# Performance work log

Hardware: AMD Instinct MI355X
Metric: run time of the kernel (lower is better)

Reference implementation:

```python
import jax, jax.numpy as jnp
import numpy as np

N_NODES = 100000
N_EDGES = 1000000
NUM_FEATURES = 64
HIDDEN = 64
NUM_GRAPHS = 128


def setup_inputs() -> dict:
    key = jax.random.key(0)
    ks = jax.random.split(key, 12)
    x = jax.random.normal(ks[0], (N_NODES, NUM_FEATURES), dtype=jnp.float32)
    edge_index = jax.random.randint(ks[1], (2, N_EDGES), 0, N_NODES, dtype=jnp.int64)
    edge_weight = jax.random.uniform(ks[2], (N_EDGES,), dtype=jnp.float32)
    batch = jnp.sort(jax.random.randint(ks[3], (N_NODES,), 0, NUM_GRAPHS, dtype=jnp.int64))
    s1 = 1.0 / np.sqrt(NUM_FEATURES)
    s2 = 1.0 / np.sqrt(HIDDEN)
    # GraphConv layer 1: lin_rel (with bias) applied to aggregated msgs, lin_root (no bias)
    w1_rel = jax.random.uniform(ks[4], (HIDDEN, NUM_FEATURES), jnp.float32, -s1, s1)
    b1_rel = jax.random.uniform(ks[5], (HIDDEN,), jnp.float32, -s1, s1)
    w1_root = jax.random.uniform(ks[6], (HIDDEN, NUM_FEATURES), jnp.float32, -s1, s1)
    # GraphConv layer 2
    w2_rel = jax.random.uniform(ks[7], (HIDDEN, HIDDEN), jnp.float32, -s2, s2)
    b2_rel = jax.random.uniform(ks[8], (HIDDEN,), jnp.float32, -s2, s2)
    w2_root = jax.random.uniform(ks[9], (HIDDEN, HIDDEN), jnp.float32, -s2, s2)
    # final Linear(hidden, 1)
    w_lin = jax.random.uniform(ks[10], (1, HIDDEN), jnp.float32, -s2, s2)
    b_lin = jax.random.uniform(ks[11], (1,), jnp.float32, -s2, s2)
    return {
        "x": x, "edge_index": edge_index, "edge_weight": edge_weight, "batch": batch,
        "w1_rel": w1_rel, "b1_rel": b1_rel, "w1_root": w1_root,
        "w2_rel": w2_rel, "b2_rel": b2_rel, "w2_root": w2_root,
        "w_lin": w_lin, "b_lin": b_lin,
    }


def graph_conv(x, edge_index, edge_weight, w_rel, b_rel, w_root):
    # messages: x[src] * e, scatter-add into dst  (gather-scale-scatter)
    src, dst = edge_index[0], edge_index[1]
    msgs = x[src] * edge_weight[:, None]                      # [E, F]
    aggr = jax.ops.segment_sum(msgs, dst, num_segments=x.shape[0])  # [N, F]
    return aggr @ w_rel.T + b_rel + x @ w_root.T


def reference(x, edge_index, edge_weight, batch,
              w1_rel, b1_rel, w1_root, w2_rel, b2_rel, w2_root, w_lin, b_lin):
    h = graph_conv(x, edge_index, edge_weight, w1_rel, b1_rel, w1_root)
    h = jax.nn.relu(h)
    h = graph_conv(h, edge_index, edge_weight, w2_rel, b2_rel, w2_root)
    # global_mean_pool over graph ids
    sums = jax.ops.segment_sum(h, batch, num_segments=NUM_GRAPHS)          # [G, H]
    counts = jax.ops.segment_sum(jnp.ones((h.shape[0],), h.dtype), batch,
                                 num_segments=NUM_GRAPHS)                  # [G]
    pooled = sums / jnp.maximum(counts, 1.0)[:, None]
    # dropout(p=0.5) in eval mode is identity
    return pooled @ w_lin.T + b_lin                                        # [G, 1]
```

## Files before the change

kernel.cpp:

```cpp
#include <hip/hip_runtime.h>
#include <hip/hip_bf16.h>


#define N_NODES 100000
#define N_EDGES 1000000
#define NGRAPHS 128
#define BN 512
#define NBUCK ((N_NODES + BN - 1) / BN)
#define FILL_T 16
#define FILL_TILE (256 * FILL_T)
#define FILL_NB ((N_EDGES + FILL_TILE - 1) / FILL_TILE)
#define NTILES (N_NODES / 16)
#define AST 72

typedef __attribute__((ext_vector_type(8))) short bf16x8;
typedef __attribute__((ext_vector_type(8))) unsigned short u16x8;
typedef __attribute__((ext_vector_type(4))) float f32x4;

__device__ __forceinline__ unsigned short f2bf(float f) {
    unsigned u = __float_as_uint(f);
    unsigned r = (u + 0x7FFFu + ((u >> 16) & 1u)) >> 16;
    return (unsigned short)r;
}
__device__ __forceinline__ float bf2f(unsigned short h) {
    return __uint_as_float(((unsigned)h) << 16);
}

__global__ __launch_bounds__(256) void prep_cvt_kernel(
    const float* __restrict__ x, unsigned short* __restrict__ xh, int n8,
    const float* __restrict__ w1rel, const float* __restrict__ w1root,
    const float* __restrict__ w2rel, const float* __restrict__ w2root,
    const float* __restrict__ wlin, const float* __restrict__ b2rel,
    const float* __restrict__ blin, unsigned short* __restrict__ whirel,
    unsigned short* __restrict__ wlorel, unsigned short* __restrict__ whiroot,
    unsigned short* __restrict__ wloroot, float* __restrict__ u,
    float* __restrict__ v, float* __restrict__ C) {
    int tid = threadIdx.x;
    int i = blockIdx.x * 256 + tid;
    if (i < n8) {
        const float4* xp = (const float4*)x + (size_t)i * 2;
        float4 a = xp[0], b = xp[1];
        u16x8 o;
        o[0] = f2bf(a.x); o[1] = f2bf(a.y); o[2] = f2bf(a.z); o[3] = f2bf(a.w);
        o[4] = f2bf(b.x); o[5] = f2bf(b.y); o[6] = f2bf(b.z); o[7] = f2bf(b.w);
        *((u16x8*)xh + i) = o;
        return;
    }
    for (int k = tid; k < 4096; k += 256) {
        float a = w1rel[k];
        unsigned short hi = f2bf(a);
        whirel[k] = hi;
        wlorel[k] = f2bf(a - bf2f(hi));
        float b = w1root[k];
        unsigned short hb = f2bf(b);
        whiroot[k] = hb;
        wloroot[k] = f2bf(b - bf2f(hb));
    }
    if (tid < 64) {
        float uu = 0.f, vv = 0.f;
        for (int h = 0; h < 64; ++h) {
            float wl = wlin[h];
            uu += wl * w2rel[h * 64 + tid];
            vv += wl * w2root[h * 64 + tid];
        }
        u[tid] = uu;
        v[tid] = vv;
    }
    if (tid == 0) {
        float c = blin[0];
        for (int h = 0; h < 64; ++h) c += wlin[h] * b2rel[h];
        *C = c;
    }
}

__global__ __launch_bounds__(256) void bucket_hist(const int* __restrict__ ei,
                                                   int* __restrict__ bcount,
                                                   int E) {
    __shared__ int lh[NBUCK];
    int tid = threadIdx.x;
    for (int i = tid; i < NBUCK; i += 256) lh[i] = 0;
    __syncthreads();
    for (int e = blockIdx.x * 256 + tid; e < E; e += gridDim.x * 256)
        atomicAdd(&lh[ei[E + e] >> 9], 1);
    __syncthreads();
    for (int i = tid; i < NBUCK; i += 256) {
        int c = lh[i];
        if (c) atomicAdd(&bcount[i], c);
    }
}

__global__ void bucket_scan(const int* __restrict__ bcount,
                            int* __restrict__ boff, int* __restrict__ cursor) {
    __shared__ int s[256];
    int t = threadIdx.x;
    int v = (t < NBUCK) ? bcount[t] : 0;
    s[t] = v;
    __syncthreads();
    for (int off = 1; off < 256; off <<= 1) {
        int x = (t >= off) ? s[t - off] : 0;
        __syncthreads();
        s[t] += x;
        __syncthreads();
    }
    if (t < NBUCK) {
        boff[t] = s[t] - v;
        cursor[t] = s[t] - v;
    }
    if (t == 255) boff[NBUCK] = s[255];
}

__global__ __launch_bounds__(256) void bucket_fill(
    const int* __restrict__ ei, const float* __restrict__ ew,
    int* __restrict__ cursor, int2* __restrict__ ebuf, int E) {
    __shared__ int lh[NBUCK];
    __shared__ int gbase[NBUCK];
    int tid = threadIdx.x;
    for (int i = tid; i < NBUCK; i += 256) lh[i] = 0;
    __syncthreads();
    int base = blockIdx.x * FILL_TILE;
    int2 rec[FILL_T];
    int meta[FILL_T];
#pragma unroll
    for (int i = 0; i < FILL_T; ++i) {
        int e = base + i * 256 + tid;
        meta[i] = -1;
        if (e < E) {
            int src = ei[e];
            int dst = ei[E + e];
            int b = dst >> 9;
            int r = atomicAdd(&lh[b], 1);
            rec[i].x = src | ((dst & (BN - 1)) << 17);
            rec[i].y = __float_as_int(ew[e]);
            meta[i] = (b << 13) | r;
        }
    }
    __syncthreads();
    for (int i = tid; i < NBUCK; i += 256) {
        int c = lh[i];
        gbase[i] = c ? atomicAdd(&cursor[i], c) : 0;
    }
    __syncthreads();
#pragma unroll
    for (int i = 0; i < FILL_T; ++i) {
        if (meta[i] >= 0) {
            int b = meta[i] >> 13;
            int r = meta[i] & 8191;
            ebuf[gbase[b] + r] = rec[i];
        }
    }
}

__global__ __launch_bounds__(512) void csr_build(
    const int* __restrict__ boff, const int2* __restrict__ ebuf,
    const int* __restrict__ batch, int* __restrict__ row_ptr,
    int2* __restrict__ csr, int N) {
    __shared__ int s[BN];
    int b = blockIdx.x;
    int t = threadIdx.x;
    int beg = boff[b], end = boff[b + 1];
    s[t] = 0;
    __syncthreads();
    for (int j = beg + t; j < end; j += 512)
        atomicAdd(&s[(ebuf[j].x >> 17) & (BN - 1)], 1);
    __syncthreads();
    int v = s[t];
    for (int off = 1; off < BN; off <<= 1) {
        int x = (t >= off) ? s[t - off] : 0;
        __syncthreads();
        s[t] += x;
        __syncthreads();
    }
    int excl = s[t] - v;
    int gidx = b * BN + t;
    if (gidx <= N) row_ptr[gidx] = beg + excl;
    __syncthreads();
    s[t] = excl;
    __syncthreads();
    for (int j = beg + t; j < end; j += 512) {
        int2 rec = ebuf[j];
        int dlo = (rec.x >> 17) & (BN - 1);
        int g = batch[b * BN + dlo];
        int r = atomicAdd(&s[dlo], 1);
        int2 o;
        o.x = (rec.x & 0x1FFFF) | (g << 17);
        o.y = rec.y;
        csr[beg + r] = o;
    }
}

__global__ __launch_bounds__(256) void gather_dense_kernel(
    const unsigned short* __restrict__ xh, const int* __restrict__ row_ptr,
    const int2* __restrict__ csr, const unsigned short* __restrict__ whirel,
    const unsigned short* __restrict__ wlorel,
    const unsigned short* __restrict__ whiroot,
    const unsigned short* __restrict__ wloroot,
    const float* __restrict__ b1rel, const float* __restrict__ u,
    const float* __restrict__ v, float* __restrict__ p, float* __restrict__ q,
    int ntiles) {
    __shared__ unsigned short arow[4][16 * AST];
    int lane = threadIdx.x & 63;
    int wv = threadIdx.x >> 6;
    int wave = (blockIdx.x << 2) + wv;
    if (wave >= ntiles) return;
    unsigned short* my = &arow[wv][0];
    int nb = wave * 16;
    int g = lane >> 4;
    int c = lane & 15;

    for (int nl = 0; nl < 16; ++nl) {
        int node = nb + nl;
        int beg = row_ptr[node], end = row_ptr[node + 1];
        float4 acc = {0.f, 0.f, 0.f, 0.f};
        for (int j0 = beg; j0 < end; j0 += 64) {
            int cnt = min(64, end - j0);
            int2 e = {0, 0};
            if (lane < cnt) e = csr[j0 + lane];
            for (int k = 0; k < cnt; k += 4) {
                int myk = k + g;
                int sj = __shfl(e.x, myk) & 0x1FFFF;
                float wj = __int_as_float(__shfl(e.y, myk));
                if (myk < cnt) {
                    ushort4 xv =
                        *(const ushort4*)(xh + (size_t)sj * 64 + c * 4);
                    acc.x += wj * bf2f(xv.x);
                    acc.y += wj * bf2f(xv.y);
                    acc.z += wj * bf2f(xv.z);
                    acc.w += wj * bf2f(xv.w);
                }
            }
        }
#pragma unroll
        for (int off = 16; off < 64; off <<= 1) {
            acc.x += __shfl_xor(acc.x, off);
            acc.y += __shfl_xor(acc.y, off);
            acc.z += __shfl_xor(acc.z, off);
            acc.w += __shfl_xor(acc.w, off);
        }
        if (lane < 16) {
            ushort4 o;
            o.x = f2bf(acc.x);
            o.y = f2bf(acc.y);
            o.z = f2bf(acc.z);
            o.w = f2bf(acc.w);
            *(ushort4*)(my + nl * AST + c * 4) = o;
        }
    }

    int lo4 = lane & 15;
    int quad = lane >> 4;
    f32x4 acc4[4];
#pragma unroll
    for (int t = 0; t < 4; ++t) acc4[t] = (f32x4){0.f, 0.f, 0.f, 0.f};
#pragma unroll
    for (int s = 0; s < 2; ++s) {
        bf16x8 Aa = *(const bf16x8*)(my + lo4 * AST + s * 32 + quad * 8);
        bf16x8 Ax = *(const bf16x8*)(xh + (size_t)(nb + lo4) * 64 + s * 32 +
                                     quad * 8);
#pragma unroll
        for (int t = 0; t < 4; ++t) {
            int off = (t * 16 + lo4) * 64 + s * 32 + quad * 8;
            bf16x8 bhr = *(const bf16x8*)(whirel + off);
            bf16x8 blr = *(const bf16x8*)(wlorel + off);
            bf16x8 bhx = *(const bf16x8*)(whiroot + off);
            bf16x8 blx = *(const bf16x8*)(wloroot + off);
            acc4[t] = __builtin_amdgcn_mfma_f32_16x16x32_bf16(Aa, bhr, acc4[t],
                                                              0, 0, 0);
            acc4[t] = __builtin_amdgcn_mfma_f32_16x16x32_bf16(Aa, blr, acc4[t],
                                                              0, 0, 0);
            acc4[t] = __builtin_amdgcn_mfma_f32_16x16x32_bf16(Ax, bhx, acc4[t],
                                                              0, 0, 0);
            acc4[t] = __builtin_amdgcn_mfma_f32_16x16x32_bf16(Ax, blx, acc4[t],
                                                              0, 0, 0);
        }
    }

    float pc[4] = {0.f, 0.f, 0.f, 0.f};
    float qc[4] = {0.f, 0.f, 0.f, 0.f};
#pragma unroll
    for (int t = 0; t < 4; ++t) {
        float bb = b1rel[t * 16 + lo4];
        float uu = u[t * 16 + lo4];
        float vv = v[t * 16 + lo4];
#pragma unroll
        for (int r = 0; r < 4; ++r) {
            float h1 = fmaxf(acc4[t][r] + bb, 0.f);
            pc[r] += uu * h1;
            qc[r] += vv * h1;
        }
    }
#pragma unroll
    for (int off = 1; off < 16; off <<= 1) {
#pragma unroll
        for (int r = 0; r < 4; ++r) {
            pc[r] += __shfl_xor(pc[r], off);
            qc[r] += __shfl_xor(qc[r], off);
        }
    }
    if (lo4 == 0) {
        f32x4 po = {pc[0], pc[1], pc[2], pc[3]};
        f32x4 qo = {qc[0], qc[1], qc[2], qc[3]};
        *(f32x4*)(p + nb + quad * 4) = po;
        *(f32x4*)(q + nb + quad * 4) = qo;
    }
}

#define PT_EPT 4
#define PT_EPW (64 * PT_EPT)
#define PT_NB ((N_EDGES + 4 * PT_EPW - 1) / (4 * PT_EPW))
#define PS_NB 98
__global__ __launch_bounds__(256) void pool_both(
    const int2* __restrict__ csr, const float* __restrict__ p,
    const float* __restrict__ q, const int* __restrict__ batch,
    float* __restrict__ gp, float* __restrict__ gq, float* __restrict__ gc,
    int E, int N) {
    __shared__ float lbuf[2 * NGRAPHS];
    int tid = threadIdx.x;
    lbuf[tid] = 0.f;
    __syncthreads();
    if (blockIdx.x < PT_NB) {
        int lane = tid & 63;
        int wid = (blockIdx.x * 256 + tid) >> 6;
        int base = wid * PT_EPW;
        float acc = 0.f;
        int curg = -1;
#pragma unroll
        for (int i = 0; i < PT_EPT; ++i) {
            int j = base + i * 64 + lane;
            if (j < E) {
                int2 e = csr[j];
                int g = ((unsigned)e.x) >> 17;
                float val = __int_as_float(e.y) * p[e.x & 0x1FFFF];
                if (g != curg) {
                    if (curg >= 0) atomicAdd(&lbuf[curg], acc);
                    curg = g;
                    acc = 0.f;
                }
                acc += val;
            }
        }
        if (curg >= 0) atomicAdd(&lbuf[curg], acc);
        __syncthreads();
        if (tid < NGRAPHS) {
            float t = lbuf[tid];
            if (t != 0.f) atomicAdd(&gp[tid], t);
        }
    } else {
        int bid = blockIdx.x - PT_NB;
        for (int i = bid * 256 + tid; i < N; i += PS_NB * 256) {
            int g = batch[i];
            atomicAdd(&lbuf[g], q[i]);
            atomicAdd(&lbuf[NGRAPHS + g], 1.f);
        }
        __syncthreads();
        if (tid < NGRAPHS) {
            if (lbuf[NGRAPHS + tid] != 0.f) {
                atomicAdd(&gq[tid], lbuf[tid]);
                atomicAdd(&gc[tid], lbuf[NGRAPHS + tid]);
            }
        }
    }
}

__global__ void final_kernel(const float* __restrict__ gp,
                             const float* __restrict__ gq,
                             const float* __restrict__ gc,
                             const float* __restrict__ C,
                             float* __restrict__ out) {
    int g = threadIdx.x;
    float c = fmaxf(gc[g], 1.0f);
    out[g] = (gp[g] + gq[g]) / c + *C;
}

extern "C" void kernel_launch(void* const* d_in, const int* in_sizes, int n_in,
                              void* d_out, int out_size, void* d_ws,
                              size_t ws_size, hipStream_t stream) {
    const float* x      = (const float*)d_in[0];
    const int*   ei     = (const int*)d_in[1];
    const float* ew     = (const float*)d_in[2];
    const int*   batch  = (const int*)d_in[3];
    const float* w1rel  = (const float*)d_in[4];
    const float* b1rel  = (const float*)d_in[5];
    const float* w1root = (const float*)d_in[6];
    const float* w2rel  = (const float*)d_in[7];
    const float* b2rel  = (const float*)d_in[8];
    const float* w2root = (const float*)d_in[9];
    const float* wlin   = (const float*)d_in[10];
    const float* blin   = (const float*)d_in[11];
    float* out = (float*)d_out;

    char* wsb = (char*)d_ws;
    int2* csr  = (int2*)wsb;
    int2* ebuf = (int2*)(wsb + (size_t)N_EDGES * 8);
    char* tail = wsb + (size_t)N_EDGES * 16;
    unsigned short* whirel  = (unsigned short*)tail;
    unsigned short* wlorel  = whirel + 4096;
    unsigned short* whiroot = wlorel + 4096;
    unsigned short* wloroot = whiroot + 4096;
    float* p  = (float*)(wloroot + 4096);
    float* q  = p + N_NODES;
    float* u  = q + N_NODES;
    float* v  = u + 64;
    float* C  = v + 64;
    int*   bcount = (int*)(C + 1);
    float* gp = (float*)(bcount + NBUCK);
    float* gq = gp + NGRAPHS;
    float* gc = gq + NGRAPHS;
    int*   boff   = (int*)(gc + NGRAPHS);
    int*   cursor = boff + (NBUCK + 1);
    int*   row_ptr = cursor + NBUCK;
    unsigned short* xh = (unsigned short*)(row_ptr + N_NODES + 2);

    hipMemsetAsync(bcount, 0, (NBUCK + 3 * NGRAPHS) * sizeof(int), stream);

    int n8 = N_NODES * 64 / 8;
    prep_cvt_kernel<<<n8 / 256 + 1, 256, 0, stream>>>(
        x, xh, n8, w1rel, w1root, w2rel, w2root, wlin, b2rel, blin, whirel,
        wlorel, whiroot, wloroot, u, v, C);

    bucket_hist<<<256, 256, 0, stream>>>(ei, bcount, N_EDGES);
    bucket_scan<<<1, 256, 0, stream>>>(bcount, boff, cursor);
    bucket_fill<<<FILL_NB, 256, 0, stream>>>(ei, ew, cursor, ebuf, N_EDGES);
    csr_build<<<NBUCK, 512, 0, stream>>>(boff, ebuf, batch, row_ptr, csr,
                                         N_NODES);

    gather_dense_kernel<<<(NTILES + 3) / 4, 256, 0, stream>>>(
        xh, row_ptr, csr, whirel, wlorel, whiroot, wloroot, b1rel, u, v, p, q,
        NTILES);

    pool_both<<<PT_NB + PS_NB, 256, 0, stream>>>(csr, p, q, batch, gp, gq, gc,
                                                 N_EDGES, N_NODES);
    final_kernel<<<1, NGRAPHS, 0, stream>>>(gp, gq, gc, C, out);
}
```

Baseline: 220.9 us.

## Fuse histogram into prep, restructure gather per node, fold final into pool

The edge-bucket histogram now runs as extra blocks of the conversion kernel, and the final output kernel is folded into the pool kernel through a last-block-done counter. Together these remove two launches. The gather phase now gives each 8-lane group its own node and has every lane load 16 bytes per neighbor with two independent accumulators. This replaces the shuffle-broadcast and cross-lane reduction scheme, but work per lane now varies with node degree, which can leave lanes in a wave idle.

New measurement: 230.5 us. 4.3% more time.

```diff
diff --git a/kernel.cpp b/kernel.cpp
--- a/kernel.cpp
+++ b/kernel.cpp
@@ -12,6 +12,8 @@
 #define FILL_NB ((N_EDGES + FILL_TILE - 1) / FILL_TILE)
 #define NTILES (N_NODES / 16)
 #define AST 72
+#define CVT_NB 3126
+#define HIST_NB 256
 
 typedef __attribute__((ext_vector_type(8))) short bf16x8;
 typedef __attribute__((ext_vector_type(8))) unsigned short u16x8;
@@ -26,7 +28,7 @@
     return __uint_as_float(((unsigned)h) << 16);
 }
 
-__global__ __launch_bounds__(256) void prep_cvt_kernel(
+__global__ __launch_bounds__(256) void prep_cvt_hist_kernel(
     const float* __restrict__ x, unsigned short* __restrict__ xh, int n8,
     const float* __restrict__ w1rel, const float* __restrict__ w1root,
     const float* __restrict__ w2rel, const float* __restrict__ w2root,
@@ -34,8 +36,23 @@
     const float* __restrict__ blin, unsigned short* __restrict__ whirel,
     unsigned short* __restrict__ wlorel, unsigned short* __restrict__ whiroot,
     unsigned short* __restrict__ wloroot, float* __restrict__ u,
-    float* __restrict__ v, float* __restrict__ C) {
+    float* __restrict__ v, float* __restrict__ C,
+    const int* __restrict__ ei, int* __restrict__ bcount, int E) {
     int tid = threadIdx.x;
+    if (blockIdx.x >= CVT_NB) {
+        __shared__ int lh[NBUCK];
+        for (int i = tid; i < NBUCK; i += 256) lh[i] = 0;
+        __syncthreads();
+        int bid2 = blockIdx.x - CVT_NB;
+        for (int e = bid2 * 256 + tid; e < E; e += HIST_NB * 256)
+            atomicAdd(&lh[ei[E + e] >> 9], 1);
+        __syncthreads();
+        for (int i = tid; i < NBUCK; i += 256) {
+            int c = lh[i];
+            if (c) atomicAdd(&bcount[i], c);
+        }
+        return;
+    }
     int i = blockIdx.x * 256 + tid;
     if (i < n8) {
         const float4* xp = (const float4*)x + (size_t)i * 2;
@@ -70,22 +87,6 @@
         float c = blin[0];
         for (int h = 0; h < 64; ++h) c += wlin[h] * b2rel[h];
         *C = c;
-    }
-}
-
-__global__ __launch_bounds__(256) void bucket_hist(const int* __restrict__ ei,
-                                                   int* __restrict__ bcount,
-                                                   int E) {
-    __shared__ int lh[NBUCK];
-    int tid = threadIdx.x;
-    for (int i = tid; i < NBUCK; i += 256) lh[i] = 0;
-    __syncthreads();
-    for (int e = blockIdx.x * 256 + tid; e < E; e += gridDim.x * 256)
-        atomicAdd(&lh[ei[E + e] >> 9], 1);
-    __syncthreads();
-    for (int i = tid; i < NBUCK; i += 256) {
-        int c = lh[i];
-        if (c) atomicAdd(&bcount[i], c);
     }
 }
 
@@ -204,46 +205,44 @@
     if (wave >= ntiles) return;
     unsigned short* my = &arow[wv][0];
     int nb = wave * 16;
-    int g = lane >> 4;
-    int c = lane & 15;
-
-    for (int nl = 0; nl < 16; ++nl) {
-        int node = nb + nl;
+    int g = lane >> 3;
+    int c = lane & 7;
+
+#pragma unroll
+    for (int r = 0; r < 2; ++r) {
+        int node = nb + r * 8 + g;
         int beg = row_ptr[node], end = row_ptr[node + 1];
-        float4 acc = {0.f, 0.f, 0.f, 0.f};
-        for (int j0 = beg; j0 < end; j0 += 64) {
-            int cnt = min(64, end - j0);
-            int2 e = {0, 0};
-            if (lane < cnt) e = csr[j0 + lane];
-            for (int k = 0; k < cnt; k += 4) {
-                int myk = k + g;
-                int sj = __shfl(e.x, myk) & 0x1FFFF;
-                float wj = __int_as_float(__shfl(e.y, myk));
-                if (myk < cnt) {
-                    ushort4 xv =
-                        *(const ushort4*)(xh + (size_t)sj * 64 + c * 4);
-                    acc.x += wj * bf2f(xv.x);
-                    acc.y += wj * bf2f(xv.y);
-                    acc.z += wj * bf2f(xv.z);
-                    acc.w += wj * bf2f(xv.w);
-                }
+        float a0[8], a1[8];
+#pragma unroll
+        for (int t = 0; t < 8; ++t) { a0[t] = 0.f; a1[t] = 0.f; }
+        int j = beg;
+        for (; j + 2 <= end; j += 2) {
+            int2 e0 = csr[j];
+            int2 e1 = csr[j + 1];
+            u16x8 x0 = *(const u16x8*)(xh + (size_t)(e0.x & 0x1FFFF) * 64 +
+                                       c * 8);
+            u16x8 x1 = *(const u16x8*)(xh + (size_t)(e1.x & 0x1FFFF) * 64 +
+                                       c * 8);
+            float w0 = __int_as_float(e0.y);
+            float w1 = __int_as_float(e1.y);
+#pragma unroll
+            for (int t = 0; t < 8; ++t) {
+                a0[t] += w0 * bf2f(x0[t]);
+                a1[t] += w1 * bf2f(x1[t]);
             }
         }
-#pragma unroll
-        for (int off = 16; off < 64; off <<= 1) {
-            acc.x += __shfl_xor(acc.x, off);
-            acc.y += __shfl_xor(acc.y, off);
-            acc.z += __shfl_xor(acc.z, off);
-            acc.w += __shfl_xor(acc.w, off);
-        }
-        if (lane < 16) {
-            ushort4 o;
-            o.x = f2bf(acc.x);
-            o.y = f2bf(acc.y);
-            o.z = f2bf(acc.z);
-            o.w = f2bf(acc.w);
-            *(ushort4*)(my + nl * AST + c * 4) = o;
-        }
+        if (j < end) {
+            int2 e0 = csr[j];
+            u16x8 x0 = *(const u16x8*)(xh + (size_t)(e0.x & 0x1FFFF) * 64 +
+                                       c * 8);
+            float w0 = __int_as_float(e0.y);
+#pragma unroll
+            for (int t = 0; t < 8; ++t) a0[t] += w0 * bf2f(x0[t]);
+        }
+        u16x8 o;
+#pragma unroll
+        for (int t = 0; t < 8; ++t) o[t] = f2bf(a0[t] + a1[t]);
+        *(u16x8*)(my + (r * 8 + g) * AST + c * 8) = o;
     }
 
     int lo4 = lane & 15;
@@ -312,8 +311,10 @@
     const int2* __restrict__ csr, const float* __restrict__ p,
     const float* __restrict__ q, const int* __restrict__ batch,
     float* __restrict__ gp, float* __restrict__ gq, float* __restrict__ gc,
-    int E, int N) {
+    int* __restrict__ done, const float* __restrict__ C,
+    float* __restrict__ out, int E, int N) {
     __shared__ float lbuf[2 * NGRAPHS];
+    __shared__ int amLast;
     int tid = threadIdx.x;
     lbuf[tid] = 0.f;
     __syncthreads();
@@ -359,16 +360,21 @@
             }
         }
     }
-}
-
-__global__ void final_kernel(const float* __restrict__ gp,
-                             const float* __restrict__ gq,
-                             const float* __restrict__ gc,
-                             const float* __restrict__ C,
-                             float* __restrict__ out) {
-    int g = threadIdx.x;
-    float c = fmaxf(gc[g], 1.0f);
-    out[g] = (gp[g] + gq[g]) / c + *C;
+    __syncthreads();
+    if (tid == 0) {
+        __threadfence();
+        amLast = (atomicAdd(done, 1) == PT_NB + PS_NB - 1);
+    }
+    __syncthreads();
+    if (amLast) {
+        __threadfence();
+        if (tid < NGRAPHS) {
+            float pv = atomicAdd(&gp[tid], 0.f);
+            float qv = atomicAdd(&gq[tid], 0.f);
+            float cv = atomicAdd(&gc[tid], 0.f);
+            out[tid] = (pv + qv) / fmaxf(cv, 1.f) + C[0];
+        }
+    }
 }
 
 extern "C" void kernel_launch(void* const* d_in, const int* in_sizes, int n_in,
@@ -405,19 +411,19 @@
     float* gp = (float*)(bcount + NBUCK);
     float* gq = gp + NGRAPHS;
     float* gc = gq + NGRAPHS;
-    int*   boff   = (int*)(gc + NGRAPHS);
+    int*   done   = (int*)(gc + NGRAPHS);
+    int*   boff   = done + 1;
     int*   cursor = boff + (NBUCK + 1);
     int*   row_ptr = cursor + NBUCK;
     unsigned short* xh = (unsigned short*)(row_ptr + N_NODES + 2);
 
-    hipMemsetAsync(bcount, 0, (NBUCK + 3 * NGRAPHS) * sizeof(int), stream);
+    hipMemsetAsync(bcount, 0, (NBUCK + 3 * NGRAPHS + 1) * sizeof(int), stream);
 
     int n8 = N_NODES * 64 / 8;
-    prep_cvt_kernel<<<n8 / 256 + 1, 256, 0, stream>>>(
+    prep_cvt_hist_kernel<<<CVT_NB + HIST_NB, 256, 0, stream>>>(
         x, xh, n8, w1rel, w1root, w2rel, w2root, wlin, b2rel, blin, whirel,
-        wlorel, whiroot, wloroot, u, v, C);
-
-    bucket_hist<<<256, 256, 0, stream>>>(ei, bcount, N_EDGES);
+        wlorel, whiroot, wloroot, u, v, C, ei, bcount, N_EDGES);
+
     bucket_scan<<<1, 256, 0, stream>>>(bcount, boff, cursor);
     bucket_fill<<<FILL_NB, 256, 0, stream>>>(ei, ew, cursor, ebuf, N_EDGES);
     csr_build<<<NBUCK, 512, 0, stream>>>(boff, ebuf, batch, row_ptr, csr,
@@ -428,6 +434,6 @@
         NTILES);
 
     pool_both<<<PT_NB + PS_NB, 256, 0, stream>>>(csr, p, q, batch, gp, gq, gc,
-                                                 N_EDGES, N_NODES);
-    final_kernel<<<1, NGRAPHS, 0, stream>>>(gp, gq, gc, C, out);
-}
+                                                 done, C, out, N_EDGES,
+                                                 N_NODES);
+}
```
